# Kernel tuning notes

Measured on AMD Instinct MI355X. Metric: run time of the kernel, lower is better.

The kernel has to match this reference:

```python
import jax, jax.numpy as jnp
import numpy as np

B, S, ENC_H, DEC_H, ATTN = 64, 2048, 512, 512, 512


def setup_inputs() -> dict:
    key = jax.random.key(0)
    k1, k2, k3, k4, k5 = jax.random.split(key, 5)
    enc_outputs = jax.random.normal(k1, (B, S, ENC_H), dtype=jnp.float32)
    dec_hidden = jax.random.normal(k2, (B, DEC_H), dtype=jnp.float32)
    # nn.Linear(in, out, bias=False): weight shape [out, in]; y = x @ W.T
    s_enc = 1.0 / np.sqrt(ENC_H)
    s_dec = 1.0 / np.sqrt(DEC_H)
    s_v = 1.0 / np.sqrt(ATTN)
    W_enc = jax.random.uniform(k3, (ATTN, ENC_H), minval=-s_enc, maxval=s_enc, dtype=jnp.float32)
    W_dec = jax.random.uniform(k4, (ATTN, DEC_H), minval=-s_dec, maxval=s_dec, dtype=jnp.float32)
    v = jax.random.uniform(k5, (1, ATTN), minval=-s_v, maxval=s_v, dtype=jnp.float32)
    return {"enc_outputs": enc_outputs, "dec_hidden": dec_hidden,
            "W_enc": W_enc, "W_dec": W_dec, "v": v}


def reference(enc_outputs, dec_hidden, W_enc, W_dec, v):
    # enc_proj: [B,S,A], dec_proj: [B,1,A]
    enc_proj = jnp.einsum('bse,ae->bsa', enc_outputs, W_enc)
    dec_proj = jnp.einsum('bd,ad->ba', dec_hidden, W_dec)[:, None, :]
    score = jnp.einsum('bsa,a->bs', jnp.tanh(enc_proj + dec_proj), v[0])  # [B,S]
    attn_weights = jax.nn.softmax(score, axis=1)
    context = jnp.einsum('bs,bse->be', attn_weights, enc_outputs)  # [B,ENC_H]
    return (context, attn_weights)
```

## Files before the change

kernel.cpp:

```cpp
#include <hip/hip_runtime.h>
#include <hip/hip_bf16.h>

#define B_N 64
#define S_N 2048
#define E_N 512
#define A_N 512

typedef __bf16 bf16x8 __attribute__((ext_vector_type(8)));
typedef float  f32x4  __attribute__((ext_vector_type(4)));

__device__ __forceinline__ unsigned int f2bfu(float f) {
  return (unsigned int)__builtin_bit_cast(unsigned short, (__bf16)f);
}

__global__ __launch_bounds__(256) void k_pack(const float* __restrict__ W,
                                              unsigned short* __restrict__ Wp) {
  const int pk = blockIdx.x * 256 + threadIdx.x;
  const int l = pk & 63, k32 = (pk >> 6) & 15, c = pk >> 10;
  const int ln = l & 15, q = l >> 4;
  const int a = c * 16 + ln, k = k32 * 32 + q * 8;
  const float* src = W + (size_t)a * E_N + k;
  const float4 u = *(const float4*)src;
  const float4 w = *(const float4*)(src + 4);
  uint4 o;
  o.x = f2bfu(u.x) | (f2bfu(u.y) << 16);
  o.y = f2bfu(u.z) | (f2bfu(u.w) << 16);
  o.z = f2bfu(w.x) | (f2bfu(w.y) << 16);
  o.w = f2bfu(w.z) | (f2bfu(w.w) << 16);
  *(uint4*)(Wp + (size_t)pk * 8) = o;
}

__global__ __launch_bounds__(256) void k_decproj(const float* __restrict__ dh,
                                                 const float* __restrict__ Wd,
                                                 float* __restrict__ decp) {
  const int b = blockIdx.x, tid = threadIdx.x;
  __shared__ float h[E_N];
  h[tid] = dh[b * E_N + tid];
  h[tid + 256] = dh[b * E_N + 256 + tid];
  __syncthreads();
  for (int a = tid; a < A_N; a += 256) {
    const float* wr = Wd + (size_t)a * E_N;
    float s = 0.f;
    #pragma unroll 8
    for (int e = 0; e < E_N; e += 4) {
      const float4 w4 = *(const float4*)(wr + e);
      s += w4.x * h[e] + w4.y * h[e + 1] + w4.z * h[e + 2] + w4.w * h[e + 3];
    }
    decp[b * A_N + a] = s;
  }
}

#define LDS_A   65536
#define RED_OFF LDS_A
#define LDS_TOT (LDS_A + 8 * 64 * 4)

__device__ __forceinline__ int a_off(int r, int kb) {
  return r * 1024 + (kb ^ ((r & 7) << 4));
}

__global__ __launch_bounds__(512, 2) void k_scores(
    const float* __restrict__ enc, const unsigned short* __restrict__ Wp,
    const float* __restrict__ decp, const float* __restrict__ vvec,
    float* __restrict__ scores) {
  __shared__ __align__(16) unsigned char lds[LDS_TOT];
  const int tid = threadIdx.x;
  const int lane = tid & 63, wv = tid >> 6, q = lane >> 4, ln = lane & 15;
  const int row0 = blockIdx.x * 64;
  const int b = row0 >> 11;
  const bf16x8* __restrict__ Wp16 = (const bf16x8*)Wp;

  float vv[4], dp[4];
  #pragma unroll
  for (int nt = 0; nt < 4; ++nt) {
    const int a = wv * 64 + nt * 16 + ln;
    vv[nt] = vvec[a];
    dp[nt] = decp[b * A_N + a];
  }

  {
    const float* srow = enc + (size_t)(row0 + wv * 8) * E_N + lane * 8;
    #pragma unroll
    for (int h = 0; h < 2; ++h) {
      float4 u[4], w4[4];
      #pragma unroll
      for (int j = 0; j < 4; ++j) {
        u[j]  = *(const float4*)(srow + (size_t)(h * 4 + j) * E_N);
        w4[j] = *(const float4*)(srow + (size_t)(h * 4 + j) * E_N + 4);
      }
      #pragma unroll
      for (int j = 0; j < 4; ++j) {
        uint4 o;
        o.x = f2bfu(u[j].x)  | (f2bfu(u[j].y)  << 16);
        o.y = f2bfu(u[j].z)  | (f2bfu(u[j].w)  << 16);
        o.z = f2bfu(w4[j].x) | (f2bfu(w4[j].y) << 16);
        o.w = f2bfu(w4[j].z) | (f2bfu(w4[j].w) << 16);
        *(uint4*)(lds + a_off(wv * 8 + h * 4 + j, lane * 16)) = o;
      }
    }
  }
  __syncthreads();

  f32x4 acc[4][4] = {};
  #pragma unroll
  for (int ks = 0; ks < 8; ++ks) {
    #pragma unroll
    for (int kt = 0; kt < 2; ++kt) {
      bf16x8 bfr[4], afr[4];
      #pragma unroll
      for (int nt = 0; nt < 4; ++nt)
        bfr[nt] = Wp16[((wv * 4 + nt) * 16 + ks * 2 + kt) * 64 + lane];
      #pragma unroll
      for (int mt = 0; mt < 4; ++mt)
        afr[mt] = *(const bf16x8*)(
            lds + a_off(mt * 16 + ln, ks * 128 + kt * 64 + q * 16));
      #pragma unroll
      for (int mt = 0; mt < 4; ++mt)
        #pragma unroll
        for (int nt = 0; nt < 4; ++nt)
          acc[mt][nt] = __builtin_amdgcn_mfma_f32_16x16x32_bf16(
              afr[mt], bfr[nt], acc[mt][nt], 0, 0, 0);
    }
  }

  float part[4][4] = {};
  #pragma unroll
  for (int mt = 0; mt < 4; ++mt)
    #pragma unroll
    for (int nt = 0; nt < 4; ++nt)
      #pragma unroll
      for (int r = 0; r < 4; ++r) {
        float x = acc[mt][nt][r] + dp[nt];
        x = fminf(9.f, fmaxf(-9.f, x));
        const float ex = __expf(2.f * x);
        part[mt][r] = fmaf(__fdividef(ex - 1.f, ex + 1.f), vv[nt], part[mt][r]);
      }
  float* red = (float*)(lds + RED_OFF);
  #pragma unroll
  for (int mt = 0; mt < 4; ++mt)
    #pragma unroll
    for (int r = 0; r < 4; ++r) {
      float s = part[mt][r];
      s += __shfl_xor(s, 1);
      s += __shfl_xor(s, 2);
      s += __shfl_xor(s, 4);
      s += __shfl_xor(s, 8);
      if (ln == 0) red[wv * 64 + mt * 16 + q * 4 + r] = s;
    }
  __syncthreads();
  if (tid < 64) {
    float s = 0.f;
    #pragma unroll
    for (int w8 = 0; w8 < 8; ++w8) s += red[w8 * 64 + tid];
    scores[row0 + tid] = s;
  }
}

__global__ __launch_bounds__(256) void k_softmax(const float* __restrict__ scores,
                                                 float* __restrict__ attn) {
  const int b = blockIdx.x, tid = threadIdx.x;
  float l[8];
  float mx = -3.4e38f;
  #pragma unroll
  for (int i = 0; i < 8; ++i) {
    l[i] = scores[b * S_N + i * 256 + tid];
    mx = fmaxf(mx, l[i]);
  }
  #pragma unroll
  for (int m = 1; m < 64; m <<= 1) mx = fmaxf(mx, __shfl_xor(mx, m));
  __shared__ float sred[8];
  if ((tid & 63) == 0) sred[tid >> 6] = mx;
  __syncthreads();
  mx = fmaxf(fmaxf(sred[0], sred[1]), fmaxf(sred[2], sred[3]));
  float se = 0.f;
  #pragma unroll
  for (int i = 0; i < 8; ++i) { l[i] = __expf(l[i] - mx); se += l[i]; }
  #pragma unroll
  for (int m = 1; m < 64; m <<= 1) se += __shfl_xor(se, m);
  if ((tid & 63) == 0) sred[4 + (tid >> 6)] = se;
  __syncthreads();
  se = sred[4] + sred[5] + sred[6] + sred[7];
  const float inv = 1.f / se;
  #pragma unroll
  for (int i = 0; i < 8; ++i) attn[b * S_N + i * 256 + tid] = l[i] * inv;
}

__global__ __launch_bounds__(512) void k_context(const float* __restrict__ enc,
                                                 const float* __restrict__ attn,
                                                 float* __restrict__ ctx) {
  const int blk = blockIdx.x;
  const int b = blk >> 2, eq = blk & 3;
  const int tid = threadIdx.x;
  const int te = tid & 31, sg = tid >> 5;
  const int e0 = eq * 128 + te * 4;
  const float* ep = enc + (size_t)b * S_N * E_N + e0;
  const float* wp = attn + b * S_N;
  f32x4 acc = {0.f, 0.f, 0.f, 0.f};
  const int s0 = sg * 128;
  #pragma unroll 4
  for (int s = s0; s < s0 + 128; ++s) {
    const float w = wp[s];
    const f32x4 ev = *(const f32x4*)(ep + (size_t)s * E_N);
    acc += w * ev;
  }
  __shared__ f32x4 red[16][32];
  red[sg][te] = acc;
  __syncthreads();
  if (sg == 0) {
    f32x4 t = red[0][te];
    #pragma unroll
    for (int g = 1; g < 16; ++g) t += red[g][te];
    *(f32x4*)(ctx + (size_t)b * E_N + e0) = t;
  }
}

extern "C" void kernel_launch(void* const* d_in, const int* in_sizes, int n_in,
                              void* d_out, int out_size, void* d_ws, size_t ws_size,
                              hipStream_t stream) {
  const float* enc = (const float*)d_in[0];
  const float* dh  = (const float*)d_in[1];
  const float* We  = (const float*)d_in[2];
  const float* Wd  = (const float*)d_in[3];
  const float* v   = (const float*)d_in[4];

  float* out_ctx  = (float*)d_out;
  float* out_attn = out_ctx + B_N * E_N;

  float* scores = (float*)d_ws;
  float* decp   = scores + B_N * S_N;
  unsigned short* Wp = (unsigned short*)(decp + B_N * A_N);

  k_pack   <<<128, 256, 0, stream>>>(We, Wp);
  k_decproj<<<B_N, 256, 0, stream>>>(dh, Wd, decp);
  k_scores <<<(B_N * S_N) / 64, 512, 0, stream>>>(enc, Wp, decp, v, scores);
  k_softmax<<<B_N, 256, 0, stream>>>(scores, out_attn);
  k_context<<<B_N * 4, 512, 0, stream>>>(enc, out_attn, out_ctx);
}
```

Measured before the change: 225.8 us.

## Split scores kernel over attention halves with double-buffered K-chunk staging

The scores kernel now splits the attention dimension across two blocks per 64-row tile, each with 4 waves, and writes two partial score arrays that the softmax kernel sums. Instead of staging the whole 64x512 bf16 tile in 64KB of LDS up front, it streams 64-column K chunks through a small double buffer, prefetching the next chunk from global memory while the MFMAs run on the current one. This cuts LDS use so more blocks fit per CU and overlaps load with compute. The cost is that the encoder rows are read twice from global memory, there is a barrier per K step, and the workspace holds an extra partial-score array.

```diff
diff --git a/kernel.cpp b/kernel.cpp
--- a/kernel.cpp
+++ b/kernel.cpp
@@ -50,69 +50,76 @@
   }
 }
 
-#define LDS_A   65536
-#define RED_OFF LDS_A
-#define LDS_TOT (LDS_A + 8 * 64 * 4)
-
-__device__ __forceinline__ int a_off(int r, int kb) {
-  return r * 1024 + (kb ^ ((r & 7) << 4));
-}
-
-__global__ __launch_bounds__(512, 2) void k_scores(
+#define LDS_ABUF 8192
+#define RED_OFF  (2 * LDS_ABUF)
+#define LDS_TOT  (2 * LDS_ABUF + 4 * 64 * 4)
+
+__device__ __forceinline__ int a_off(int pb, int r, int kb) {
+  return pb * LDS_ABUF + r * 128 + (kb ^ ((r & 7) << 4));
+}
+
+__global__ __launch_bounds__(256, 4) void k_scores(
     const float* __restrict__ enc, const unsigned short* __restrict__ Wp,
     const float* __restrict__ decp, const float* __restrict__ vvec,
-    float* __restrict__ scores) {
+    float* __restrict__ sp) {
   __shared__ __align__(16) unsigned char lds[LDS_TOT];
   const int tid = threadIdx.x;
-  const int lane = tid & 63, wv = tid >> 6, q = lane >> 4, ln = lane & 15;
-  const int row0 = blockIdx.x * 64;
-  const int b = row0 >> 11;
+  const int lane = tid & 63, w = tid >> 6, q = lane >> 4, ln = lane & 15;
+  const int g = blockIdx.x >> 1, p = blockIdx.x & 1;
+  const int m0 = g * 64;
+  const int b = m0 >> 11;
   const bf16x8* __restrict__ Wp16 = (const bf16x8*)Wp;
 
   float vv[4], dp[4];
   #pragma unroll
   for (int nt = 0; nt < 4; ++nt) {
-    const int a = wv * 64 + nt * 16 + ln;
+    const int a = p * 256 + w * 64 + nt * 16 + ln;
     vv[nt] = vvec[a];
     dp[nt] = decp[b * A_N + a];
   }
 
+  const int srow = tid >> 2, c4 = tid & 3;
+  const float* sbase = enc + (size_t)(m0 + srow) * E_N + c4 * 16;
+
   {
-    const float* srow = enc + (size_t)(row0 + wv * 8) * E_N + lane * 8;
+    float4 L[4];
+    #pragma unroll
+    for (int j = 0; j < 4; ++j) L[j] = *(const float4*)(sbase + j * 4);
     #pragma unroll
     for (int h = 0; h < 2; ++h) {
-      float4 u[4], w4[4];
-      #pragma unroll
-      for (int j = 0; j < 4; ++j) {
-        u[j]  = *(const float4*)(srow + (size_t)(h * 4 + j) * E_N);
-        w4[j] = *(const float4*)(srow + (size_t)(h * 4 + j) * E_N + 4);
-      }
-      #pragma unroll
-      for (int j = 0; j < 4; ++j) {
-        uint4 o;
-        o.x = f2bfu(u[j].x)  | (f2bfu(u[j].y)  << 16);
-        o.y = f2bfu(u[j].z)  | (f2bfu(u[j].w)  << 16);
-        o.z = f2bfu(w4[j].x) | (f2bfu(w4[j].y) << 16);
-        o.w = f2bfu(w4[j].z) | (f2bfu(w4[j].w) << 16);
-        *(uint4*)(lds + a_off(wv * 8 + h * 4 + j, lane * 16)) = o;
-      }
+      uint4 o;
+      o.x = f2bfu(L[h*2].x)   | (f2bfu(L[h*2].y)   << 16);
+      o.y = f2bfu(L[h*2].z)   | (f2bfu(L[h*2].w)   << 16);
+      o.z = f2bfu(L[h*2+1].x) | (f2bfu(L[h*2+1].y) << 16);
+      o.w = f2bfu(L[h*2+1].z) | (f2bfu(L[h*2+1].w) << 16);
+      *(uint4*)(lds + a_off(0, srow, c4 * 32 + h * 16)) = o;
     }
   }
   __syncthreads();
 
   f32x4 acc[4][4] = {};
-  #pragma unroll
+
+  #pragma unroll 1
   for (int ks = 0; ks < 8; ++ks) {
+    const int pb = ks & 1;
+    float4 L[4];
+    if (ks < 7) {
+      #pragma unroll
+      for (int j = 0; j < 4; ++j)
+        L[j] = *(const float4*)(sbase + (ks + 1) * 64 + j * 4);
+    }
     #pragma unroll
     for (int kt = 0; kt < 2; ++kt) {
       bf16x8 bfr[4], afr[4];
       #pragma unroll
-      for (int nt = 0; nt < 4; ++nt)
-        bfr[nt] = Wp16[((wv * 4 + nt) * 16 + ks * 2 + kt) * 64 + lane];
+      for (int nt = 0; nt < 4; ++nt) {
+        const int c = p * 16 + w * 4 + nt;
+        bfr[nt] = Wp16[(size_t)(c * 16 + ks * 2 + kt) * 64 + lane];
+      }
       #pragma unroll
       for (int mt = 0; mt < 4; ++mt)
         afr[mt] = *(const bf16x8*)(
-            lds + a_off(mt * 16 + ln, ks * 128 + kt * 64 + q * 16));
+            lds + a_off(pb, mt * 16 + ln, kt * 64 + q * 16));
       #pragma unroll
       for (int mt = 0; mt < 4; ++mt)
         #pragma unroll
@@ -120,6 +127,18 @@
           acc[mt][nt] = __builtin_amdgcn_mfma_f32_16x16x32_bf16(
               afr[mt], bfr[nt], acc[mt][nt], 0, 0, 0);
     }
+    if (ks < 7) {
+      #pragma unroll
+      for (int h = 0; h < 2; ++h) {
+        uint4 o;
+        o.x = f2bfu(L[h*2].x)   | (f2bfu(L[h*2].y)   << 16);
+        o.y = f2bfu(L[h*2].z)   | (f2bfu(L[h*2].w)   << 16);
+        o.z = f2bfu(L[h*2+1].x) | (f2bfu(L[h*2+1].y) << 16);
+        o.w = f2bfu(L[h*2+1].z) | (f2bfu(L[h*2+1].w) << 16);
+        *(uint4*)(lds + a_off(pb ^ 1, srow, c4 * 32 + h * 16)) = o;
+      }
+    }
+    __syncthreads();
   }
 
   float part[4][4] = {};
@@ -144,25 +163,24 @@
       s += __shfl_xor(s, 2);
       s += __shfl_xor(s, 4);
       s += __shfl_xor(s, 8);
-      if (ln == 0) red[wv * 64 + mt * 16 + q * 4 + r] = s;
+      if (ln == 0) red[w * 64 + mt * 16 + q * 4 + r] = s;
     }
   __syncthreads();
   if (tid < 64) {
-    float s = 0.f;
-    #pragma unroll
-    for (int w8 = 0; w8 < 8; ++w8) s += red[w8 * 64 + tid];
-    scores[row0 + tid] = s;
-  }
-}
-
-__global__ __launch_bounds__(256) void k_softmax(const float* __restrict__ scores,
+    const float s = red[tid] + red[64 + tid] + red[128 + tid] + red[192 + tid];
+    sp[p * (B_N * S_N) + m0 + tid] = s;
+  }
+}
+
+__global__ __launch_bounds__(256) void k_softmax(const float* __restrict__ sp,
                                                  float* __restrict__ attn) {
   const int b = blockIdx.x, tid = threadIdx.x;
   float l[8];
   float mx = -3.4e38f;
   #pragma unroll
   for (int i = 0; i < 8; ++i) {
-    l[i] = scores[b * S_N + i * 256 + tid];
+    const int idx = b * S_N + i * 256 + tid;
+    l[i] = sp[idx] + sp[B_N * S_N + idx];
     mx = fmaxf(mx, l[i]);
   }
   #pragma unroll
@@ -225,13 +243,13 @@
   float* out_ctx  = (float*)d_out;
   float* out_attn = out_ctx + B_N * E_N;
 
-  float* scores = (float*)d_ws;
-  float* decp   = scores + B_N * S_N;
+  float* sp   = (float*)d_ws;
+  float* decp = sp + 2 * B_N * S_N;
   unsigned short* Wp = (unsigned short*)(decp + B_N * A_N);
 
   k_pack   <<<128, 256, 0, stream>>>(We, Wp);
   k_decproj<<<B_N, 256, 0, stream>>>(dh, Wd, decp);
-  k_scores <<<(B_N * S_N) / 64, 512, 0, stream>>>(enc, Wp, decp, v, scores);
-  k_softmax<<<B_N, 256, 0, stream>>>(scores, out_attn);
+  k_scores <<<(B_N * S_N) / 64 * 2, 256, 0, stream>>>(enc, Wp, decp, v, sp);
+  k_softmax<<<B_N, 256, 0, stream>>>(sp, out_attn);
   k_context<<<B_N * 4, 512, 0, stream>>>(enc, out_attn, out_ctx);
 }
```

After: 385.2 us. 1.71x slower.

## Double-buffer encoder and weight tiles through LDS with async global-to-LDS loads

Applied to the files above, without the earlier changes.

The scores kernel now streams K in 64-wide slices, double-buffering both the bf16 encoder tile and the packed W_enc slice in LDS. The W slice is copied with global_load_lds, and the next slice's loads overlap the MFMAs on the current one. Previously each wave read its B fragments straight from global memory, and the whole 64x512 A tile was staged once up front. The weight pack layout is reordered to match the new per-slice layout. The new version uses about 146KB of LDS per block, which allows only one 512-thread block per CU, and it adds a barrier per K slice.

```diff
diff --git a/kernel.cpp b/kernel.cpp
--- a/kernel.cpp
+++ b/kernel.cpp
@@ -5,23 +5,37 @@
 #define S_N 2048
 #define E_N 512
 #define A_N 512
+#define SPN (B_N * S_N)
 
 typedef __bf16 bf16x8 __attribute__((ext_vector_type(8)));
 typedef float  f32x4  __attribute__((ext_vector_type(4)));
 
 __device__ __forceinline__ unsigned int f2bfu(float f) {
   return (unsigned int)__builtin_bit_cast(unsigned short, (__bf16)f);
+}
+
+__device__ __forceinline__ float tanh_term(float x) {
+  x = fminf(9.f, fmaxf(-9.f, x));
+  const float ex = __expf(2.f * x);
+  return __fdividef(ex - 1.f, ex + 1.f);
+}
+
+__device__ __forceinline__ void gl16(const void* g, void* l) {
+  __builtin_amdgcn_global_load_lds(
+      (const __attribute__((address_space(1))) unsigned int*)g,
+      (__attribute__((address_space(3))) unsigned int*)l, 16, 0, 0);
 }
 
 __global__ __launch_bounds__(256) void k_pack(const float* __restrict__ W,
                                               unsigned short* __restrict__ Wp) {
   const int pk = blockIdx.x * 256 + threadIdx.x;
-  const int l = pk & 63, k32 = (pk >> 6) & 15, c = pk >> 10;
-  const int ln = l & 15, q = l >> 4;
-  const int a = c * 16 + ln, k = k32 * 32 + q * 8;
+  const int l = pk & 63, cb = (pk >> 6) & 63, ks = pk >> 12;
+  const int c16 = cb >> 1, kt = cb & 1;
+  const int a = c16 * 16 + (l & 15);
+  const int k = ks * 64 + kt * 32 + (l >> 4) * 8;
   const float* src = W + (size_t)a * E_N + k;
-  const float4 u = *(const float4*)src;
-  const float4 w = *(const float4*)(src + 4);
+  const f32x4 u = *(const f32x4*)src;
+  const f32x4 w = *(const f32x4*)(src + 4);
   uint4 o;
   o.x = f2bfu(u.x) | (f2bfu(u.y) << 16);
   o.y = f2bfu(u.z) | (f2bfu(u.w) << 16);
@@ -50,69 +64,71 @@
   }
 }
 
-#define LDS_A   65536
-#define RED_OFF LDS_A
-#define LDS_TOT (LDS_A + 8 * 64 * 4)
-
-__device__ __forceinline__ int a_off(int r, int kb) {
-  return r * 1024 + (kb ^ ((r & 7) << 4));
-}
-
-__global__ __launch_bounds__(512, 2) void k_scores(
+__global__ __launch_bounds__(512) void k_scores(
     const float* __restrict__ enc, const unsigned short* __restrict__ Wp,
     const float* __restrict__ decp, const float* __restrict__ vvec,
     float* __restrict__ scores) {
-  __shared__ __align__(16) unsigned char lds[LDS_TOT];
+  __shared__ __align__(16) unsigned char ldsA[2 * 8192];
+  __shared__ __align__(16) unsigned char ldsB[2 * 65536];
+  __shared__ float red[8][64];
   const int tid = threadIdx.x;
   const int lane = tid & 63, wv = tid >> 6, q = lane >> 4, ln = lane & 15;
   const int row0 = blockIdx.x * 64;
   const int b = row0 >> 11;
-  const bf16x8* __restrict__ Wp16 = (const bf16x8*)Wp;
+  const unsigned char* WpB = (const unsigned char*)Wp;
 
   float vv[4], dp[4];
   #pragma unroll
   for (int nt = 0; nt < 4; ++nt) {
-    const int a = wv * 64 + nt * 16 + ln;
-    vv[nt] = vvec[a];
-    dp[nt] = decp[b * A_N + a];
-  }
+    const int col = wv * 64 + nt * 16 + ln;
+    vv[nt] = vvec[col];
+    dp[nt] = decp[b * A_N + col];
+  }
+
+  const float* aSrc =
+      enc + (size_t)(row0 + (wv >> 1) * 16 + ln) * E_N + (wv & 1) * 32 + q * 8;
+  unsigned char* aDst = ldsA + wv * 1024 + lane * 16;
 
   {
-    const float* srow = enc + (size_t)(row0 + wv * 8) * E_N + lane * 8;
-    #pragma unroll
-    for (int h = 0; h < 2; ++h) {
-      float4 u[4], w4[4];
-      #pragma unroll
-      for (int j = 0; j < 4; ++j) {
-        u[j]  = *(const float4*)(srow + (size_t)(h * 4 + j) * E_N);
-        w4[j] = *(const float4*)(srow + (size_t)(h * 4 + j) * E_N + 4);
-      }
-      #pragma unroll
-      for (int j = 0; j < 4; ++j) {
-        uint4 o;
-        o.x = f2bfu(u[j].x)  | (f2bfu(u[j].y)  << 16);
-        o.y = f2bfu(u[j].z)  | (f2bfu(u[j].w)  << 16);
-        o.z = f2bfu(w4[j].x) | (f2bfu(w4[j].y) << 16);
-        o.w = f2bfu(w4[j].z) | (f2bfu(w4[j].w) << 16);
-        *(uint4*)(lds + a_off(wv * 8 + h * 4 + j, lane * 16)) = o;
-      }
-    }
+    const f32x4 a0 = *(const f32x4*)(aSrc);
+    const f32x4 a1 = *(const f32x4*)(aSrc + 4);
+    #pragma unroll
+    for (int i = 0; i < 8; ++i)
+      gl16(WpB + (size_t)(wv * 8 + i) * 1024 + lane * 16,
+           ldsB + (wv * 8 + i) * 1024);
+    uint4 o;
+    o.x = f2bfu(a0.x) | (f2bfu(a0.y) << 16);
+    o.y = f2bfu(a0.z) | (f2bfu(a0.w) << 16);
+    o.z = f2bfu(a1.x) | (f2bfu(a1.y) << 16);
+    o.w = f2bfu(a1.z) | (f2bfu(a1.w) << 16);
+    *(uint4*)aDst = o;
   }
   __syncthreads();
 
   f32x4 acc[4][4] = {};
-  #pragma unroll
+  #pragma unroll 1
   for (int ks = 0; ks < 8; ++ks) {
+    const int buf = ks & 1;
+    f32x4 a0, a1;
+    if (ks < 7) {
+      a0 = *(const f32x4*)(aSrc + (ks + 1) * 64);
+      a1 = *(const f32x4*)(aSrc + (ks + 1) * 64 + 4);
+      #pragma unroll
+      for (int i = 0; i < 8; ++i)
+        gl16(WpB + (size_t)((ks + 1) * 64 + wv * 8 + i) * 1024 + lane * 16,
+             ldsB + (buf ^ 1) * 65536 + (wv * 8 + i) * 1024);
+    }
     #pragma unroll
     for (int kt = 0; kt < 2; ++kt) {
-      bf16x8 bfr[4], afr[4];
-      #pragma unroll
-      for (int nt = 0; nt < 4; ++nt)
-        bfr[nt] = Wp16[((wv * 4 + nt) * 16 + ks * 2 + kt) * 64 + lane];
+      bf16x8 afr[4], bfr[4];
       #pragma unroll
       for (int mt = 0; mt < 4; ++mt)
         afr[mt] = *(const bf16x8*)(
-            lds + a_off(mt * 16 + ln, ks * 128 + kt * 64 + q * 16));
+            ldsA + buf * 8192 + (mt * 2 + kt) * 1024 + lane * 16);
+      #pragma unroll
+      for (int nt = 0; nt < 4; ++nt)
+        bfr[nt] = *(const bf16x8*)(
+            ldsB + buf * 65536 + ((wv * 4 + nt) * 2 + kt) * 1024 + lane * 16);
       #pragma unroll
       for (int mt = 0; mt < 4; ++mt)
         #pragma unroll
@@ -120,37 +136,37 @@
           acc[mt][nt] = __builtin_amdgcn_mfma_f32_16x16x32_bf16(
               afr[mt], bfr[nt], acc[mt][nt], 0, 0, 0);
     }
-  }
-
-  float part[4][4] = {};
-  #pragma unroll
-  for (int mt = 0; mt < 4; ++mt)
-    #pragma unroll
-    for (int nt = 0; nt < 4; ++nt)
-      #pragma unroll
-      for (int r = 0; r < 4; ++r) {
-        float x = acc[mt][nt][r] + dp[nt];
-        x = fminf(9.f, fmaxf(-9.f, x));
-        const float ex = __expf(2.f * x);
-        part[mt][r] = fmaf(__fdividef(ex - 1.f, ex + 1.f), vv[nt], part[mt][r]);
-      }
-  float* red = (float*)(lds + RED_OFF);
-  #pragma unroll
-  for (int mt = 0; mt < 4; ++mt)
+    if (ks < 7) {
+      uint4 o;
+      o.x = f2bfu(a0.x) | (f2bfu(a0.y) << 16);
+      o.y = f2bfu(a0.z) | (f2bfu(a0.w) << 16);
+      o.z = f2bfu(a1.x) | (f2bfu(a1.y) << 16);
+      o.w = f2bfu(a1.z) | (f2bfu(a1.w) << 16);
+      *(uint4*)(aDst + (buf ^ 1) * 8192) = o;
+    }
+    __syncthreads();
+  }
+
+  #pragma unroll
+  for (int mt = 0; mt < 4; ++mt) {
     #pragma unroll
     for (int r = 0; r < 4; ++r) {
-      float s = part[mt][r];
+      float s = 0.f;
+      #pragma unroll
+      for (int nt = 0; nt < 4; ++nt)
+        s = fmaf(tanh_term(acc[mt][nt][r] + dp[nt]), vv[nt], s);
       s += __shfl_xor(s, 1);
       s += __shfl_xor(s, 2);
       s += __shfl_xor(s, 4);
       s += __shfl_xor(s, 8);
-      if (ln == 0) red[wv * 64 + mt * 16 + q * 4 + r] = s;
-    }
+      if (ln == 0) red[wv][mt * 16 + q * 4 + r] = s;
+    }
+  }
   __syncthreads();
   if (tid < 64) {
     float s = 0.f;
     #pragma unroll
-    for (int w8 = 0; w8 < 8; ++w8) s += red[w8 * 64 + tid];
+    for (int w8 = 0; w8 < 8; ++w8) s += red[w8][tid];
     scores[row0 + tid] = s;
   }
 }
@@ -226,12 +242,12 @@
   float* out_attn = out_ctx + B_N * E_N;
 
   float* scores = (float*)d_ws;
-  float* decp   = scores + B_N * S_N;
+  float* decp   = scores + SPN;
   unsigned short* Wp = (unsigned short*)(decp + B_N * A_N);
 
   k_pack   <<<128, 256, 0, stream>>>(We, Wp);
   k_decproj<<<B_N, 256, 0, stream>>>(dh, Wd, decp);
-  k_scores <<<(B_N * S_N) / 64, 512, 0, stream>>>(enc, Wp, decp, v, scores);
+  k_scores <<<SPN / 64, 512, 0, stream>>>(enc, Wp, decp, v, scores);
   k_softmax<<<B_N, 256, 0, stream>>>(scores, out_attn);
   k_context<<<B_N * 4, 512, 0, stream>>>(enc, out_attn, out_ctx);
 }
```

After: 256.8 us. +13.7%, slower.
